# Performance work log

Measured on AMD Instinct MI355X. Metric: run time of the kernel, lower is better.

The kernel has to match this reference:

```python
import jax, jax.numpy as jnp
import numpy as np

NUM_CLASSES = 1000
FEAT_DIM = 512
BATCH = 32768
LAMDA = 0.5
EPS = 1e-8  # torch cosine_similarity denominator clamp


def setup_inputs() -> dict:
    key = jax.random.key(0)
    k1, k2, k3 = jax.random.split(key, 3)
    label = jax.random.randint(k1, (BATCH,), 0, NUM_CLASSES, dtype=jnp.int64 if jax.config.jax_enable_x64 else jnp.int32)
    feat = jax.random.normal(k2, (BATCH, FEAT_DIM), dtype=jnp.float32)
    centers = jax.random.normal(k3, (NUM_CLASSES, FEAT_DIM), dtype=jnp.float32)
    return {"label": label, "feat": feat, "centers": centers}


def reference(label, feat, centers):
    # center loss: gather per-sample center, squared distance, size-averaged
    centers_batch = centers[label]                      # [B, D] gather
    center_loss = jnp.sum((feat - centers_batch) ** 2) / 2.0 / BATCH

    # island loss: sum over ordered pairs j != k of (cos(c_j, c_k) + 1)
    # vectorized as normalized Gram matrix with off-diagonal masked sum
    norms = jnp.maximum(jnp.linalg.norm(centers, axis=1, keepdims=True), EPS)
    cn = centers / norms                                # [N, D]
    gram = cn @ cn.T                                    # [N, N] cosine sims
    off_diag = ~jnp.eye(NUM_CLASSES, dtype=bool)
    island_loss = jnp.sum(jnp.where(off_diag, gram + 1.0, 0.0))

    return center_loss + LAMDA * island_loss
```

## Files before the change

### kernel.cpp

```cpp
#include <hip/hip_runtime.h>
#include <math.h>

#define NUM_CLASSES 1000
#define FEAT_DIM    512
#define BATCH       32768
#define LAMDA       0.5f
#define EPS         1e-8f

#define SB   25
#define CB   2023
#define GRID (SB + CB)
#define ROWS_PER_BLOCK 40
#define TOTAL4  (BATCH * FEAT_DIM / 4)
#define STRIDE  (CB * 256)

#define DIAG_OFF 25600
#define CL_OFF   26624


__global__ __launch_bounds__(256, 8) void k_main(const float* __restrict__ feat,
                                                 const float* __restrict__ centers,
                                                 const int* __restrict__ label,
                                                 float* __restrict__ ws) {
    __shared__ float s_sh[4][512];
    __shared__ float d_sh[4];
    __shared__ float sm[4];
    const int t = threadIdx.x;
    const int w = t >> 6, l = t & 63;

    if (blockIdx.x < SB) {
        const float4* c4 = (const float4*)centers;
        const int j0 = blockIdx.x * ROWS_PER_BLOCK;
        float4 sa = make_float4(0.f, 0.f, 0.f, 0.f);
        float4 sb = make_float4(0.f, 0.f, 0.f, 0.f);
        float diag = 0.f;
        for (int r = w; r < ROWS_PER_BLOCK; r += 4) {
            const int j = j0 + r;
            const float4 a = c4[j * 128 + l];
            const float4 b = c4[j * 128 + 64 + l];
            float n2 = a.x*a.x + a.y*a.y + a.z*a.z + a.w*a.w
                     + b.x*b.x + b.y*b.y + b.z*b.z + b.w*b.w;
            for (int o = 32; o > 0; o >>= 1) n2 += __shfl_xor(n2, o, 64);
            const float inv = 1.0f / fmaxf(sqrtf(n2), EPS);
            sa.x += a.x * inv; sa.y += a.y * inv; sa.z += a.z * inv; sa.w += a.w * inv;
            sb.x += b.x * inv; sb.y += b.y * inv; sb.z += b.z * inv; sb.w += b.w * inv;
            diag += n2 * inv * inv;
        }
        s_sh[w][4*l+0] = sa.x; s_sh[w][4*l+1] = sa.y;
        s_sh[w][4*l+2] = sa.z; s_sh[w][4*l+3] = sa.w;
        s_sh[w][256+4*l+0] = sb.x; s_sh[w][256+4*l+1] = sb.y;
        s_sh[w][256+4*l+2] = sb.z; s_sh[w][256+4*l+3] = sb.w;
        if (l == 0) d_sh[w] = diag;
        __syncthreads();
        const float v0 = s_sh[0][t] + s_sh[1][t] + s_sh[2][t] + s_sh[3][t];
        const float v1 = s_sh[0][t+256] + s_sh[1][t+256] + s_sh[2][t+256] + s_sh[3][t+256];
        ws[blockIdx.x * 512 + t]       = v0;
        ws[blockIdx.x * 512 + 256 + t] = v1;
        if (t == 0)
            ws[DIAG_OFF + blockIdx.x] = d_sh[0] + d_sh[1] + d_sh[2] + d_sh[3];
    } else {
        const float4* f4 = (const float4*)feat;
        const float4* c4 = (const float4*)centers;
        const int tid = (blockIdx.x - SB) * 256 + t;

        int lab[9];
#pragma unroll
        for (int k = 0; k < 8; ++k)
            lab[k] = label[(tid + k * STRIDE) >> 7];
        const int idx8 = tid + 8 * STRIDE;
        lab[8] = (idx8 < TOTAL4) ? label[idx8 >> 7] : 0;

        float acc = 0.f;
#pragma unroll
        for (int k = 0; k < 8; ++k) {
            const int idx = tid + k * STRIDE;
            const float4 f = f4[idx];
            const float4 c = c4[lab[k] * 128 + (idx & 127)];
            const float dx = f.x - c.x, dy = f.y - c.y,
                        dz = f.z - c.z, dw = f.w - c.w;
            acc += dx * dx + dy * dy + dz * dz + dw * dw;
        }
        if (idx8 < TOTAL4) {
            const float4 f = f4[idx8];
            const float4 c = c4[lab[8] * 128 + (idx8 & 127)];
            const float dx = f.x - c.x, dy = f.y - c.y,
                        dz = f.z - c.z, dw = f.w - c.w;
            acc += dx * dx + dy * dy + dz * dz + dw * dw;
        }
        for (int o = 32; o > 0; o >>= 1) acc += __shfl_down(acc, o, 64);
        if (l == 0) sm[w] = acc;
        __syncthreads();
        if (t == 0) ws[CL_OFF + (blockIdx.x - SB)] = sm[0] + sm[1] + sm[2] + sm[3];
    }
}

__global__ __launch_bounds__(1024) void k_final(const float* __restrict__ ws,
                                                float* __restrict__ out) {
    __shared__ float sm[16];
    const int t = threadIdx.x;
    const int w = t >> 6, l = t & 63;

    float island = 0.f;
    if (t < 128) {
        float4 sq = make_float4(0.f, 0.f, 0.f, 0.f);
#pragma unroll
        for (int bb = 0; bb < SB; ++bb) {
            const float4 p = ((const float4*)(ws + bb * FEAT_DIM))[t];
            sq.x += p.x; sq.y += p.y; sq.z += p.z; sq.w += p.w;
        }
        island = sq.x*sq.x + sq.y*sq.y + sq.z*sq.z + sq.w*sq.w;
    } else if (t < 128 + SB) {
        island = -ws[DIAG_OFF + (t - 128)];
    }

    float cl = ws[CL_OFF + t < CL_OFF + CB ? CL_OFF + t : CL_OFF];
    cl = (t < CB) ? ws[CL_OFF + t] : 0.f;
    if (t + 1024 < CB) cl += ws[CL_OFF + t + 1024];

    float val = LAMDA * island + cl * (0.5f / (float)BATCH);

    for (int o = 32; o > 0; o >>= 1) val += __shfl_down(val, o, 64);
    if (l == 0) sm[w] = val;
    __syncthreads();
    if (w == 0) {
        float v = (l < 16) ? sm[l] : 0.f;
        for (int o = 8; o > 0; o >>= 1) v += __shfl_down(v, o, 64);
        if (l == 0)
            out[0] = v + LAMDA * (float)NUM_CLASSES * (float)(NUM_CLASSES - 1);
    }
}

extern "C" void kernel_launch(void* const* d_in, const int* in_sizes, int n_in,
                              void* d_out, int out_size, void* d_ws, size_t ws_size,
                              hipStream_t stream) {
    const int*   label   = (const int*)d_in[0];
    const float* feat    = (const float*)d_in[1];
    const float* centers = (const float*)d_in[2];
    float* ws  = (float*)d_ws;
    float* out = (float*)d_out;

    k_main<<<GRID, 256, 0, stream>>>(feat, centers, label, ws);
    k_final<<<1, 1024, 0, stream>>>(ws, out);
}
```

Before: 21.18 us.

## Assign contiguous feature slabs per block and reorder center-loss blocks first

Center-loss blocks now each process a contiguous 4096-float4 slab with 16 unrolled loads per thread, replacing the grid-strided layout across 2023 blocks. This cuts the block count to 1024, which makes the final reduction simpler. The 25 island-loss blocks move to the end of the grid, and the occupancy hint drops from 8 to 4 blocks per CU. More loads stay in flight per thread and label reads become more local. The cost is higher register pressure and fewer, longer blocks, which could leave tail imbalance.

```diff
diff --git a/kernel.cpp b/kernel.cpp
--- a/kernel.cpp
+++ b/kernel.cpp
@@ -7,18 +7,19 @@
 #define LAMDA       0.5f
 #define EPS         1e-8f
 
+#define CB   1024
 #define SB   25
-#define CB   2023
-#define GRID (SB + CB)
+#define GRID (CB + SB)
 #define ROWS_PER_BLOCK 40
 #define TOTAL4  (BATCH * FEAT_DIM / 4)
-#define STRIDE  (CB * 256)
+#define SLAB    4096
+#define NCHUNK  16
 
 #define DIAG_OFF 25600
 #define CL_OFF   26624
 
 
-__global__ __launch_bounds__(256, 8) void k_main(const float* __restrict__ feat,
+__global__ __launch_bounds__(256, 4) void k_main(const float* __restrict__ feat,
                                                  const float* __restrict__ centers,
                                                  const int* __restrict__ label,
                                                  float* __restrict__ ws) {
@@ -28,9 +29,34 @@
     const int t = threadIdx.x;
     const int w = t >> 6, l = t & 63;
 
-    if (blockIdx.x < SB) {
+    if (blockIdx.x < CB) {
+        const float4* f4 = (const float4*)feat;
         const float4* c4 = (const float4*)centers;
-        const int j0 = blockIdx.x * ROWS_PER_BLOCK;
+        const int base = blockIdx.x * SLAB + t;
+
+        int lab[NCHUNK];
+#pragma unroll
+        for (int k = 0; k < NCHUNK; ++k)
+            lab[k] = label[(base + k * 256) >> 7];
+
+        float acc = 0.f;
+#pragma unroll
+        for (int k = 0; k < NCHUNK; ++k) {
+            const int idx = base + k * 256;
+            const float4 f = f4[idx];
+            const float4 c = c4[lab[k] * 128 + (idx & 127)];
+            const float dx = f.x - c.x, dy = f.y - c.y,
+                        dz = f.z - c.z, dw = f.w - c.w;
+            acc += dx * dx + dy * dy + dz * dz + dw * dw;
+        }
+        for (int o = 32; o > 0; o >>= 1) acc += __shfl_down(acc, o, 64);
+        if (l == 0) sm[w] = acc;
+        __syncthreads();
+        if (t == 0) ws[CL_OFF + blockIdx.x] = sm[0] + sm[1] + sm[2] + sm[3];
+    } else {
+        const float4* c4 = (const float4*)centers;
+        const int sbid = blockIdx.x - CB;
+        const int j0 = sbid * ROWS_PER_BLOCK;
         float4 sa = make_float4(0.f, 0.f, 0.f, 0.f);
         float4 sb = make_float4(0.f, 0.f, 0.f, 0.f);
         float diag = 0.f;
@@ -54,43 +80,10 @@
         __syncthreads();
         const float v0 = s_sh[0][t] + s_sh[1][t] + s_sh[2][t] + s_sh[3][t];
         const float v1 = s_sh[0][t+256] + s_sh[1][t+256] + s_sh[2][t+256] + s_sh[3][t+256];
-        ws[blockIdx.x * 512 + t]       = v0;
-        ws[blockIdx.x * 512 + 256 + t] = v1;
+        ws[sbid * 512 + t]       = v0;
+        ws[sbid * 512 + 256 + t] = v1;
         if (t == 0)
-            ws[DIAG_OFF + blockIdx.x] = d_sh[0] + d_sh[1] + d_sh[2] + d_sh[3];
-    } else {
-        const float4* f4 = (const float4*)feat;
-        const float4* c4 = (const float4*)centers;
-        const int tid = (blockIdx.x - SB) * 256 + t;
-
-        int lab[9];
-#pragma unroll
-        for (int k = 0; k < 8; ++k)
-            lab[k] = label[(tid + k * STRIDE) >> 7];
-        const int idx8 = tid + 8 * STRIDE;
-        lab[8] = (idx8 < TOTAL4) ? label[idx8 >> 7] : 0;
-
-        float acc = 0.f;
-#pragma unroll
-        for (int k = 0; k < 8; ++k) {
-            const int idx = tid + k * STRIDE;
-            const float4 f = f4[idx];
-            const float4 c = c4[lab[k] * 128 + (idx & 127)];
-            const float dx = f.x - c.x, dy = f.y - c.y,
-                        dz = f.z - c.z, dw = f.w - c.w;
-            acc += dx * dx + dy * dy + dz * dz + dw * dw;
-        }
-        if (idx8 < TOTAL4) {
-            const float4 f = f4[idx8];
-            const float4 c = c4[lab[8] * 128 + (idx8 & 127)];
-            const float dx = f.x - c.x, dy = f.y - c.y,
-                        dz = f.z - c.z, dw = f.w - c.w;
-            acc += dx * dx + dy * dy + dz * dz + dw * dw;
-        }
-        for (int o = 32; o > 0; o >>= 1) acc += __shfl_down(acc, o, 64);
-        if (l == 0) sm[w] = acc;
-        __syncthreads();
-        if (t == 0) ws[CL_OFF + (blockIdx.x - SB)] = sm[0] + sm[1] + sm[2] + sm[3];
+            ws[DIAG_OFF + sbid] = d_sh[0] + d_sh[1] + d_sh[2] + d_sh[3];
     }
 }
 
@@ -113,10 +106,7 @@
         island = -ws[DIAG_OFF + (t - 128)];
     }
 
-    float cl = ws[CL_OFF + t < CL_OFF + CB ? CL_OFF + t : CL_OFF];
-    cl = (t < CB) ? ws[CL_OFF + t] : 0.f;
-    if (t + 1024 < CB) cl += ws[CL_OFF + t + 1024];
-
+    const float cl = ws[CL_OFF + t];
     float val = LAMDA * island + cl * (0.5f / (float)BATCH);
 
     for (int o = 32; o > 0; o >>= 1) val += __shfl_down(val, o, 64);
```

Result: slower. 23.74 us (+12.1%).
